# Kernel tuning notes

Hardware: AMD Instinct MI355X
Metric: run time of the kernel (lower is better)

## Reference

```python
import jax, jax.numpy as jnp
import numpy as np

B, S, SE = 4, 1024, 1024
E, H, M = 768, 12, 100
D = E // H
EPS = 1e-5
GELU_C = 0.7978845608028654  # sqrt(2/pi)


def _ln(x, g, b):
    mu = x.mean(-1, keepdims=True)
    v = ((x - mu) ** 2).mean(-1, keepdims=True)
    return g * (x - mu) / jnp.sqrt(v + EPS) + b


def _gelu(x):
    return 0.5 * x * (1.0 + jnp.tanh(GELU_C * (x + 0.044715 * x ** 3)))


def _split(x):  # [b,s,E] -> [b,H,s,D]
    b, s, _ = x.shape
    return x.reshape(b, s, H, D).transpose(0, 2, 1, 3)


def _merge(x):  # [b,H,s,D] -> [b,s,E]
    b, h, s, d = x.shape
    return x.transpose(0, 2, 1, 3).reshape(b, s, h * d)


def _forward(x, encoder_features, ln1_g, ln1_b, ln2_g, ln2_b,
             c_attn_w, c_attn_b, attn_proj_w, attn_proj_b,
             memory_features, mem_attn_w, mem_attn_b, mem_alpha_w, mem_alpha_b,
             fcq_w, fcq_b, fck_w, fck_b, fcv_w, fcv_b, enc_proj_w, enc_proj_b,
             fc_alpha1_w, fc_alpha1_b, fc_alpha2_w, fc_alpha2_b,
             mlp_fc_w, mlp_fc_b, mlp_proj_w, mlp_proj_b, mask_encoder):
    # ---- memory-augmented self-attention (note: original has NO 1/sqrt(d) scaling here) ----
    h = _ln(x, ln1_g, ln1_b)
    qkv = h @ c_attn_w + c_attn_b
    q, k, v = jnp.split(qkv, 3, axis=-1)
    q, k, v = _split(q), _split(k), _split(v)
    w = jax.nn.softmax(jnp.einsum('bhqd,bhkd->bhqk', q, k), axis=-1)
    a = _merge(jnp.einsum('bhqk,bhkd->bhqd', w, v))
    # memory slots are batch-independent -> compute once, broadcast over batch
    mem = memory_features[0] @ mem_attn_w + mem_attn_b  # [M, 2E]
    mk, mv = jnp.split(mem, 2, axis=-1)
    mk = mk.reshape(M, H, D).transpose(1, 2, 0)  # [H,D,M]
    mv = mv.reshape(M, H, D).transpose(1, 0, 2)  # [H,M,D]
    wm = jax.nn.softmax(jnp.einsum('bhqd,hdm->bhqm', q, mk), axis=-1)
    a1 = _merge(jnp.einsum('bhqm,hmd->bhqd', wm, mv))
    al = jax.nn.sigmoid(jnp.concatenate([a, a1], -1) @ mem_alpha_w + mem_alpha_b)
    a = al * a + (1.0 - al) * a1
    a = a @ attn_proj_w + attn_proj_b
    a = x + a  # residual (dropout = identity in eval)

    # ---- two cross-attentions sharing weights and ln_1 ----
    ha = _ln(a, ln1_g, ln1_b)

    def enc_dec(enc):
        qe = _split(ha @ fcq_w + fcq_b)
        ke = _split(enc @ fck_w + fck_b)
        ve = _split(enc @ fcv_w + fcv_b)
        we = jnp.einsum('bhqd,bhkd->bhqk', qe, ke) / np.float32(np.sqrt(D))
        we = jnp.where(mask_encoder, jnp.float32(-10000.0), we)
        we = jax.nn.softmax(we, axis=-1)
        o = _merge(jnp.einsum('bhqk,bhkd->bhqd', we, ve))
        return o @ enc_proj_w + enc_proj_b

    e1 = enc_dec(_ln(encoder_features[:, 0], ln1_g, ln1_b))
    e2 = enc_dec(_ln(encoder_features[:, 1], ln1_g, ln1_b))
    al1 = jax.nn.sigmoid(jnp.concatenate([a, e1], -1) @ fc_alpha1_w + fc_alpha1_b)
    al2 = jax.nn.sigmoid(jnp.concatenate([a, e2], -1) @ fc_alpha2_w + fc_alpha2_b)
    e1 = al1 * a + (1.0 - al1) * e1
    e2 = al2 * a + (1.0 - al2) * e2
    a = (e1 + e2) / np.float32(np.sqrt(2.0))

    # ---- MLP ----
    hm = _ln(a, ln2_g, ln2_b)
    m = _gelu(hm @ mlp_fc_w + mlp_fc_b) @ mlp_proj_w + mlp_proj_b
    return a + m


def setup_inputs() -> dict:
    key = jax.random.key(0)
    ks = iter(jax.random.split(key, 48))

    def rn(shape, s=0.02):
        return jax.random.normal(next(ks), shape, jnp.float32) * s

    return dict(
        x=jax.random.normal(next(ks), (B, S, E), jnp.float32),
        encoder_features=jax.random.normal(next(ks), (B, 2, SE, E), jnp.float32),
        mask_encoder=jax.random.bernoulli(next(ks), 0.1, (B, 1, 1, SE)),
        ln1_g=jnp.ones(E, jnp.float32), ln1_b=jnp.zeros(E, jnp.float32),
        ln2_g=jnp.ones(E, jnp.float32), ln2_b=jnp.zeros(E, jnp.float32),
        c_attn_w=rn((E, 3 * E)), c_attn_b=jnp.zeros(3 * E, jnp.float32),
        attn_proj_w=rn((E, E)), attn_proj_b=jnp.zeros(E, jnp.float32),
        memory_features=rn((1, M, E), 1.0),
        mem_attn_w=rn((E, 2 * E)), mem_attn_b=jnp.zeros(2 * E, jnp.float32),
        mem_alpha_w=rn((2 * E, E)), mem_alpha_b=jnp.zeros(E, jnp.float32),
        fcq_w=rn((E, E)), fcq_b=jnp.zeros(E, jnp.float32),
        fck_w=rn((E, E)), fck_b=jnp.zeros(E, jnp.float32),
        fcv_w=rn((E, E)), fcv_b=jnp.zeros(E, jnp.float32),
        enc_proj_w=rn((E, E)), enc_proj_b=jnp.zeros(E, jnp.float32),
        fc_alpha1_w=rn((2 * E, E)), fc_alpha1_b=jnp.zeros(E, jnp.float32),
        fc_alpha2_w=rn((2 * E, E)), fc_alpha2_b=jnp.zeros(E, jnp.float32),
        mlp_fc_w=rn((E, 4 * E)), mlp_fc_b=jnp.zeros(4 * E, jnp.float32),
        mlp_proj_w=rn((4 * E, E)), mlp_proj_b=jnp.zeros(E, jnp.float32),
    )


def reference(x, encoder_features, mask_encoder, ln1_g, ln1_b, ln2_g, ln2_b,
              c_attn_w, c_attn_b, attn_proj_w, attn_proj_b,
              memory_features, mem_attn_w, mem_attn_b, mem_alpha_w, mem_alpha_b,
              fcq_w, fcq_b, fck_w, fck_b, fcv_w, fcv_b, enc_proj_w, enc_proj_b,
              fc_alpha1_w, fc_alpha1_b, fc_alpha2_w, fc_alpha2_b,
              mlp_fc_w, mlp_fc_b, mlp_proj_w, mlp_proj_b):
    return _forward(x, encoder_features, ln1_g, ln1_b, ln2_g, ln2_b,
                    c_attn_w, c_attn_b, attn_proj_w, attn_proj_b,
                    memory_features, mem_attn_w, mem_attn_b, mem_alpha_w, mem_alpha_b,
                    fcq_w, fcq_b, fck_w, fck_b, fcv_w, fcv_b, enc_proj_w, enc_proj_b,
                    fc_alpha1_w, fc_alpha1_b, fc_alpha2_w, fc_alpha2_b,
                    mlp_fc_w, mlp_fc_b, mlp_proj_w, mlp_proj_b, mask_encoder)
```

## Files before the change

### kernel.cpp

```cpp
#include <hip/hip_runtime.h>

typedef __bf16 bf16_t;
typedef __bf16 bf16x8v __attribute__((ext_vector_type(8)));
typedef float f32x4 __attribute__((ext_vector_type(4)));

#define CB 4
#define CE 768
#define CH 12
#define CD 64

__device__ __forceinline__ float fexp2(float x) { return __builtin_amdgcn_exp2f(x); }

__device__ __forceinline__ void gload16(const void* g, void* l) {
    __builtin_amdgcn_global_load_lds((const __attribute__((address_space(1))) void*)g,
                                     (__attribute__((address_space(3))) void*)l, 16, 0, 0);
}

__device__ __forceinline__ void xcd_remap(int& bx, int& by, int gx, int gy) {
    int nwg = gx * gy;
    if ((nwg & 7) == 0) {
        int lin = by * gx + bx;
        int lin2 = (lin & 7) * (nwg >> 3) + (lin >> 3);
        bx = lin2 % gx;
        by = lin2 / gx;
    }
}

template<int BM, int BN, int CONCAT, int ACT, int RES, int OUT, int CMODE>
__global__ __launch_bounds__(256)
void gemm_n(const bf16_t* __restrict__ A0, const bf16_t* __restrict__ A1,
            const bf16_t* __restrict__ Bt, const float* __restrict__ bias,
            const float* __restrict__ bias2, const void* __restrict__ resid,
            void* __restrict__ C, void* __restrict__ C2, void* __restrict__ C3,
            int M, int N, int K, int lda, int ldc)
{
    constexpr int WM = BM / 2, WN = BN / 2, RM = WM / 16, RN = WN / 16;
    __shared__ __align__(16) bf16_t As0[BM * 64], As1[BM * 64];
    __shared__ __align__(16) bf16_t Bs0[BN * 64], Bs1[BN * 64];

    const int t = threadIdx.x;
    const int lane = t & 63, wave = t >> 6;
    int bx = blockIdx.x, by = blockIdx.y;
    xcd_remap(bx, by, gridDim.x, gridDim.y);
    const int m0 = by * BM, n0 = bx * BN;
    const int wm = (wave & 1) * WM, wn = (wave >> 1) * WN;
    const int fr = lane & 15, quad = lane >> 4;

    const int lr = lane >> 3;
    const int kof = ((lane & 7) ^ lr) * 8;

    const bf16_t* A1b = A1;
    if (CMODE == 6) A1b = A1 + (n0 >= 768 ? (long)4096 * 768 : 0);

    f32x4 acc[RM][RN];
#pragma unroll
    for (int i = 0; i < RM; i++)
#pragma unroll
        for (int j = 0; j < RN; j++)
#pragma unroll
            for (int p = 0; p < 4; p++) acc[i][j][p] = 0.f;

    auto stage = [&](bf16_t* As, bf16_t* Bs, int kt) {
        const bf16_t* Ab = A0;
        int kk = kt;
        if (CONCAT && kt >= 768) { Ab = A1b; kk = kt - 768; }
        const bf16_t* asrc = Ab + (long)(m0 + wave * 8 + lr) * lda + kk + kof;
#pragma unroll
        for (int c = 0; c < BM / 32; ++c)
            gload16(asrc + (long)c * 32 * lda, &As[(c * 32 + wave * 8) * 64]);
        const bf16_t* bsrc = Bt + (long)(n0 + wave * 8 + lr) * K + kt + kof;
#pragma unroll
        for (int c = 0; c < BN / 32; ++c)
            gload16(bsrc + (long)c * 32 * K, &Bs[(c * 32 + wave * 8) * 64]);
    };

    const int sw = fr & 7;
    auto compute = [&](const bf16_t* As, const bf16_t* Bs) {
        bf16x8v af[RM][2], bfr[RN][2];
        const int s0 = quad ^ sw;
#pragma unroll
        for (int i = 0; i < RM; ++i) {
            const char* rb = (const char*)As + (wm + i * 16 + fr) * 128;
            af[i][0] = *(const bf16x8v*)(rb + (s0 << 4));
            af[i][1] = *(const bf16x8v*)(rb + ((s0 ^ 4) << 4));
        }
#pragma unroll
        for (int j = 0; j < RN; ++j) {
            const char* rb = (const char*)Bs + (wn + j * 16 + fr) * 128;
            bfr[j][0] = *(const bf16x8v*)(rb + (s0 << 4));
            bfr[j][1] = *(const bf16x8v*)(rb + ((s0 ^ 4) << 4));
        }
#pragma unroll
        for (int ks = 0; ks < 2; ++ks)
#pragma unroll
            for (int i = 0; i < RM; ++i)
#pragma unroll
                for (int j = 0; j < RN; ++j)
                    acc[i][j] = __builtin_amdgcn_mfma_f32_16x16x32_bf16(af[i][ks], bfr[j][ks], acc[i][j], 0, 0, 0);
    };

    const int nk = K >> 6;
    stage(As0, Bs0, 0);
    __syncthreads();
    for (int kt = 0; kt + 2 <= nk; kt += 2) {
        stage(As1, Bs1, (kt + 1) << 6);
        compute(As0, Bs0);
        __syncthreads();
        if (kt + 2 < nk) stage(As0, Bs0, (kt + 2) << 6);
        compute(As1, Bs1);
        __syncthreads();
    }

    const int rq = quad * 4, cn = fr;
#pragma unroll
    for (int i = 0; i < RM; i++)
#pragma unroll
        for (int j = 0; j < RN; j++) {
            int col = n0 + wn + j * 16 + cn;
            int t3 = (CMODE == 4 || CMODE == 5) ? (col / 768) : 0;
            int cc = col - t3 * 768;
            float bv = 0.f;
            if (CMODE == 5)      bv = t3 ? bias2[cc] : bias[cc];
            else if (CMODE == 6) bv = (col < 768) ? bias[col] : bias2[col - 768];
            else if (bias)       bv = bias[col];
            const int row0 = m0 + wm + i * 16 + rq;
            float vv[4];
#pragma unroll
            for (int p = 0; p < 4; p++) {
                float v = acc[i][j][p] + bv;
                if (ACT == 1) v = 1.f / (1.f + __expf(-v));
                if (ACT == 2) {
                    float u2 = 1.5957691216057308f * (v + 0.044715f * v * v * v);
                    v = v / (1.f + __expf(-u2));
                }
                if (RES == 2) v += ((const float*)resid)[(long)(row0 + p) * ldc + col];
                vv[p] = v;
            }
            if (CMODE == 0) {
#pragma unroll
                for (int p = 0; p < 4; p++) {
                    long idx = (long)(row0 + p) * ldc + col;
                    if (OUT == 0)      ((bf16_t*)C)[idx] = (bf16_t)vv[p];
                    else if (OUT == 1) ((float*)C)[idx] = vv[p];
                    else { ((float*)C)[idx] = vv[p]; ((bf16_t*)C2)[idx] = (bf16_t)vv[p]; }
                }
            } else if (CMODE == 6) {
                long base = (col < 768) ? 0 : ((long)4096 * 768 - 768);
#pragma unroll
                for (int p = 0; p < 4; p++)
                    ((bf16_t*)C)[base + (long)(row0 + p) * 768 + col] = (bf16_t)vv[p];
            } else {
                int bb = row0 >> 10, ss0 = row0 & 1023;
                int hh = cc >> 6, dd = cc & 63;
                long srow = (long)(bb * CH + hh) * 1024 + ss0;
                long tbase = (((long)(bb * CH + hh) * 64) + dd) * 1024 + ss0;
                union { ushort4 u4; bf16_t b[4]; } pk;
#pragma unroll
                for (int p = 0; p < 4; p++) pk.b[p] = (bf16_t)vv[p];
                if (CMODE == 2) {
#pragma unroll
                    for (int p = 0; p < 4; p++)
                        ((bf16_t*)C)[(srow + p) * 64 + dd] = pk.b[p];
                } else if (CMODE == 5) {
                    if (t3 == 0) {
#pragma unroll
                        for (int p = 0; p < 4; p++)
                            ((bf16_t*)C)[(srow + p) * 64 + dd] = pk.b[p];
                    } else {
                        *(ushort4*)((bf16_t*)C2 + tbase) = pk.u4;
                    }
                } else {
                    if (t3 == 0) {
#pragma unroll
                        for (int p = 0; p < 4; p++)
                            ((bf16_t*)C)[(srow + p) * 64 + dd] = pk.b[p];
                    } else if (t3 == 1) {
#pragma unroll
                        for (int p = 0; p < 4; p++)
                            ((bf16_t*)C2)[(srow + p) * 64 + dd] = pk.b[p];
                    } else {
                        *(ushort4*)((bf16_t*)C3 + tbase) = pk.u4;
                    }
                }
            }
        }
}

template<int MODE>
__global__ __launch_bounds__(256)
void flash_attn(const bf16_t* __restrict__ Q, const bf16_t* __restrict__ K,
                const bf16_t* __restrict__ V, const int* __restrict__ mask,
                bf16_t* __restrict__ O)
{
    __shared__ __align__(16) bf16_t Qs[64 * 72];
    __shared__ __align__(16) bf16_t Ks0[64 * 64], Ks1[64 * 64];
    __shared__ __align__(16) bf16_t Vs[64 * 64];

    const int t = threadIdx.x;
    const int lane = t & 63, wave = t >> 6;
    int bx = blockIdx.x, bz = blockIdx.z;
    {
        int nwg = gridDim.x * gridDim.z;
        if ((nwg & 7) == 0) {
            int lin = bz * gridDim.x + bx;
            int lin2 = (lin & 7) * (nwg >> 3) + (lin >> 3);
            bx = lin2 % gridDim.x;
            bz = lin2 / gridDim.x;
        }
    }
    const int zq = (MODE == 1) ? (bz % 48) : bz;
    const int b = zq / CH, h = bz % CH;
    const long eoff = (MODE == 1) ? (long)(bz / 48) * ((long)4096 * 768) : 0;
    const int q0 = bx * 64;

    const bf16_t* Qb = Q + (long)zq * 65536 + (long)q0 * 64;
    const bf16_t* Kb = (MODE == 2) ? K + (long)h * (128 * 64) : K + (long)bz * 65536;
    const bf16_t* Vb = (MODE == 2) ? V + (long)h * (64 * 128) : V + (long)bz * 65536;
    const int ldv = (MODE == 2) ? 128 : 1024;
    const int NT = (MODE == 2) ? 2 : 16;
    constexpr float SCL = (MODE == 1) ? 0.18033688011112042f : 1.4426950408889634f;

    const int lr = lane >> 3, kof = ((lane & 7) ^ lr) * 8;

    auto stageK = [&](bf16_t* Ks, int kt) {
#pragma unroll
        for (int c = 0; c < 2; ++c) {
            int r = wave * 8 + c * 32;
            gload16(Kb + (long)(kt * 64 + r + lr) * 64 + kof, &Ks[r * 64]);
        }
    };
    auto stageV = [&](int kt) {
#pragma unroll
        for (int c = 0; c < 2; ++c) {
            int r = wave * 8 + c * 32;
            gload16(Vb + (long)(r + lr) * ldv + kt * 64 + kof, &Vs[r * 64]);
        }
    };

    stageK(Ks0, 0);
    const int r0 = t >> 3, c0 = (t & 7) * 8;
    for (int rr = r0; rr < 64; rr += 32)
        *(uint4*)&Qs[rr * 72 + c0] = *(const uint4*)&Qb[(long)rr * 64 + c0];
    __syncthreads();

    const int fr = lane & 15, quad = lane >> 4;
    const int sw = fr & 7;
    bf16x8v qf[2];
#pragma unroll
    for (int ks = 0; ks < 2; ks++) {
        bf16x8v raw = *(const bf16x8v*)&Qs[(wave * 16 + fr) * 72 + quad * 8 + ks * 32];
#pragma unroll
        for (int i = 0; i < 8; i++) qf[ks][i] = (bf16_t)((float)raw[i] * SCL);
    }

    bf16_t* Ps = &Qs[wave * 16 * 72];

    f32x4 o[4];
    float mrow = -1e30f, lrow = 0.f;
#pragma unroll
    for (int j = 0; j < 4; j++)
#pragma unroll
        for (int p = 0; p < 4; p++) o[j][p] = 0.f;

    auto qkt_sm = [&](const bf16_t* Ks, int kt) {
        f32x4 s[4];
#pragma unroll
        for (int j = 0; j < 4; j++)
#pragma unroll
            for (int p = 0; p < 4; p++) s[j][p] = 0.f;
        __builtin_amdgcn_s_setprio(1);
#pragma unroll
        for (int ks = 0; ks < 2; ks++) {
            bf16x8v bk[4];
#pragma unroll
            for (int j = 0; j < 4; j++) {
                const char* rb = (const char*)Ks + (j * 16 + fr) * 128;
                bk[j] = *(const bf16x8v*)(rb + (((quad ^ sw) ^ (ks << 2)) << 4));
            }
#pragma unroll
            for (int j = 0; j < 4; j++)
                s[j] = __builtin_amdgcn_mfma_f32_16x16x32_bf16(bk[j], qf[ks], s[j], 0, 0, 0);
        }
        __builtin_amdgcn_s_setprio(0);
        if (MODE == 1) {
#pragma unroll
            for (int j = 0; j < 4; j++) {
                int4 mv = *(const int4*)&mask[(long)b * 1024 + kt * 64 + j * 16 + quad * 4];
                s[j][0] = mv.x ? -14426.95f : s[j][0];
                s[j][1] = mv.y ? -14426.95f : s[j][1];
                s[j][2] = mv.z ? -14426.95f : s[j][2];
                s[j][3] = mv.w ? -14426.95f : s[j][3];
            }
        }
        if (MODE == 2) {
#pragma unroll
            for (int j = 0; j < 4; j++)
#pragma unroll
                for (int p = 0; p < 4; p++)
                    if (kt * 64 + j * 16 + quad * 4 + p >= 100) s[j][p] = -1e30f;
        }
        float tm = s[0][0];
#pragma unroll
        for (int j = 0; j < 4; j++)
#pragma unroll
            for (int p = 0; p < 4; p++) tm = fmaxf(tm, s[j][p]);
        tm = fmaxf(tm, __shfl_xor(tm, 16, 64));
        tm = fmaxf(tm, __shfl_xor(tm, 32, 64));
        bool need = tm > mrow + 8.f;
        if (__any(need ? 1 : 0)) {
            float mnew = fmaxf(mrow, tm);
            float alpha = fexp2(mrow - mnew);
            lrow *= alpha;
            mrow = mnew;
            float arow[4];
#pragma unroll
            for (int p = 0; p < 4; p++)
                arow[p] = __shfl(alpha, (lane & 48) | (quad * 4 + p), 64);
#pragma unroll
            for (int j = 0; j < 4; j++)
#pragma unroll
                for (int p = 0; p < 4; p++) o[j][p] *= arow[p];
        }
        float rs = 0.f;
#pragma unroll
        for (int j = 0; j < 4; j++)
#pragma unroll
            for (int p = 0; p < 4; p++) {
                float e = fexp2(s[j][p] - mrow);
                s[j][p] = e;
                rs += e;
            }
        rs += __shfl_xor(rs, 16, 64);
        rs += __shfl_xor(rs, 32, 64);
        lrow += rs;
#pragma unroll
        for (int j = 0; j < 4; j++) {
            union { uint2 u; bf16_t bb[4]; } pk;
#pragma unroll
            for (int p = 0; p < 4; p++) pk.bb[p] = (bf16_t)s[j][p];
            *(uint2*)&Ps[fr * 72 + j * 16 + quad * 4] = pk.u;
        }
    };

    auto pv = [&]() {
        __builtin_amdgcn_s_setprio(1);
#pragma unroll
        for (int ks = 0; ks < 2; ks++) {
            bf16x8v af = *(const bf16x8v*)&Ps[fr * 72 + quad * 8 + ks * 32];
            bf16x8v bv[4];
#pragma unroll
            for (int j = 0; j < 4; j++) {
                const char* rb = (const char*)Vs + (j * 16 + fr) * 128;
                bv[j] = *(const bf16x8v*)(rb + (((quad ^ sw) ^ (ks << 2)) << 4));
            }
#pragma unroll
            for (int j = 0; j < 4; j++)
                o[j] = __builtin_amdgcn_mfma_f32_16x16x32_bf16(af, bv[j], o[j], 0, 0, 0);
        }
        __builtin_amdgcn_s_setprio(0);
    };

    for (int kt = 0; kt < NT; kt += 2) {
        stageV(kt);
        if (kt + 1 < NT) stageK(Ks1, kt + 1);
        qkt_sm(Ks0, kt);
        __syncthreads();
        pv();
        __syncthreads();
        stageV(kt + 1);
        if (kt + 2 < NT) stageK(Ks0, kt + 2);
        qkt_sm(Ks1, kt + 1);
        __syncthreads();
        pv();
        __syncthreads();
    }
    float linv[4];
#pragma unroll
    for (int p = 0; p < 4; p++)
        linv[p] = 1.f / __shfl(lrow, (lane & 48) | (quad * 4 + p), 64);
#pragma unroll
    for (int p = 0; p < 4; p++) {
        int srow = q0 + wave * 16 + quad * 4 + p;
        long base = ((long)b * 1024 + srow) * 768 + h * 64 + eoff;
#pragma unroll
        for (int j = 0; j < 4; j++)
            O[base + j * 16 + fr] = (bf16_t)(o[j][p] * linv[p]);
    }
}

__device__ __forceinline__ void ln_body(const float* in, bf16_t* out,
                                        const float* g, const float* b,
                                        long base, long ob, int t)
{
    __shared__ float red[4];
    float v0 = in[base + t], v1 = in[base + t + 256], v2 = in[base + t + 512];
    float s = v0 + v1 + v2;
    for (int m = 32; m; m >>= 1) s += __shfl_xor(s, m, 64);
    if ((t & 63) == 0) red[t >> 6] = s;
    __syncthreads();
    s = red[0] + red[1] + red[2] + red[3];
    __syncthreads();
    const float mu = s * (1.f / 768.f);
    float d0 = v0 - mu, d1 = v1 - mu, d2 = v2 - mu;
    float q = d0 * d0 + d1 * d1 + d2 * d2;
    for (int m = 32; m; m >>= 1) q += __shfl_xor(q, m, 64);
    if ((t & 63) == 0) red[t >> 6] = q;
    __syncthreads();
    q = red[0] + red[1] + red[2] + red[3];
    const float rstd = rsqrtf(q * (1.f / 768.f) + 1e-5f);
    out[ob + t]       = (bf16_t)(g[t]       * d0 * rstd + b[t]);
    out[ob + t + 256] = (bf16_t)(g[t + 256] * d1 * rstd + b[t + 256]);
    out[ob + t + 512] = (bf16_t)(g[t + 512] * d2 * rstd + b[t + 512]);
}

__global__ __launch_bounds__(256)
void ln_kernel(const float* __restrict__ in, bf16_t* __restrict__ out,
               const float* __restrict__ g, const float* __restrict__ b)
{
    const int r = blockIdx.x;
    ln_body(in, out, g, b, (long)r * CE, (long)r * CE, threadIdx.x);
}

__global__ __launch_bounds__(256)
void ln_enc(const float* __restrict__ encf, bf16_t* __restrict__ out,
            const float* __restrict__ g, const float* __restrict__ b)
{
    const int r = blockIdx.x;
    const int e = r >> 12, rr = r & 4095, bb = rr >> 10, s = rr & 1023;
    ln_body(encf, out, g, b, ((long)(bb * 2 + e) * 1024 + s) * CE, (long)r * CE, threadIdx.x);
}

__global__ void blend_kernel(const bf16_t* __restrict__ al, bf16_t* __restrict__ a,
                             const bf16_t* __restrict__ a1)
{
    int idx = blockIdx.x * 256 + threadIdx.x;
    float g = (float)al[idx];
    a[idx] = (bf16_t)(g * (float)a[idx] + (1.f - g) * (float)a1[idx]);
}

__global__ void fuse_gates2(const bf16_t* __restrict__ gal, const bf16_t* __restrict__ eo,
                            float* __restrict__ rf)
{
    const long SZel = (long)4096 * 768;
    long idx = (long)blockIdx.x * 256 + threadIdx.x;
    float g1 = (float)gal[idx], g2 = (float)gal[idx + SZel];
    float e1 = (float)eo[idx],  e2 = (float)eo[idx + SZel];
    float r = rf[idx];
    float v = g1 * r + (1.f - g1) * e1 + g2 * r + (1.f - g2) * e2;
    rf[idx] = v * 0.7071067811865476f;
}

__global__ void zero_out(float* __restrict__ out)
{
    out[blockIdx.x * 256 + threadIdx.x] = 0.f;
}

__global__ void transpose_cast(const float* __restrict__ in, bf16_t* __restrict__ out,
                               int K, int N)
{
    __shared__ bf16_t tile[32][33];
    int n0 = blockIdx.x * 32, k0 = blockIdx.y * 32;
    int tx = threadIdx.x, ty = threadIdx.y;
    for (int i = ty; i < 32; i += 8)
        tile[i][tx] = (bf16_t)in[(long)(k0 + i) * N + n0 + tx];
    __syncthreads();
    for (int i = ty; i < 32; i += 8)
        out[(long)(n0 + i) * K + k0 + tx] = tile[tx][i];
}

__global__ void cast_pad_mem(const float* __restrict__ memf, bf16_t* __restrict__ out)
{
    int idx = blockIdx.x * 256 + threadIdx.x;
    int row = idx / 768;
    out[idx] = (row < 100) ? (bf16_t)memf[idx] : (bf16_t)0.f;
}

__global__ void repack_mem(const bf16_t* __restrict__ mem, bf16_t* __restrict__ mkt,
                           bf16_t* __restrict__ mvt)
{
    int idx = blockIdx.x * 256 + threadIdx.x;
    int d = idx & 63;
    int slot = (idx >> 6) & 127;
    int h = idx >> 13;
    bf16_t kv = (slot < 100) ? mem[slot * 1536 + h * CD + d] : (bf16_t)0.f;
    bf16_t vv = (slot < 100) ? mem[slot * 1536 + CE + h * CD + d] : (bf16_t)0.f;
    mkt[idx] = kv;
    mvt[((long)h * 64 + d) * 128 + slot] = vv;
}

extern "C" void kernel_launch(void* const* d_in, const int* in_sizes, int n_in,
                              void* d_out, int out_size, void* d_ws, size_t ws_size,
                              hipStream_t stream)
{
    (void)in_sizes; (void)n_in; (void)out_size;
    const float* x        = (const float*)d_in[0];
    const float* encf     = (const float*)d_in[1];
    const int*   maskenc  = (const int*)d_in[2];
    const float* ln1_g    = (const float*)d_in[3];
    const float* ln1_b    = (const float*)d_in[4];
    const float* ln2_g    = (const float*)d_in[5];
    const float* ln2_b    = (const float*)d_in[6];
    const float* c_attn_w = (const float*)d_in[7];
    const float* c_attn_b = (const float*)d_in[8];
    const float* aproj_w  = (const float*)d_in[9];
    const float* aproj_b  = (const float*)d_in[10];
    const float* memf     = (const float*)d_in[11];
    const float* mattn_w  = (const float*)d_in[12];
    const float* mattn_b  = (const float*)d_in[13];
    const float* malpha_w = (const float*)d_in[14];
    const float* malpha_b = (const float*)d_in[15];
    const float* fcq_w    = (const float*)d_in[16];
    const float* fcq_b    = (const float*)d_in[17];
    const float* fck_w    = (const float*)d_in[18];
    const float* fck_b    = (const float*)d_in[19];
    const float* fcv_w    = (const float*)d_in[20];
    const float* fcv_b    = (const float*)d_in[21];
    const float* eproj_w  = (const float*)d_in[22];
    const float* eproj_b  = (const float*)d_in[23];
    const float* fa1_w    = (const float*)d_in[24];
    const float* fa1_b    = (const float*)d_in[25];
    const float* fa2_w    = (const float*)d_in[26];
    const float* fa2_b    = (const float*)d_in[27];
    const float* mfc_w    = (const float*)d_in[28];
    const float* mfc_b    = (const float*)d_in[29];
    const float* mproj_w  = (const float*)d_in[30];
    const float* mproj_b  = (const float*)d_in[31];
    float* dout = (float*)d_out;

    size_t off = 0;
    auto alloc = [&](size_t bytes) -> void* {
        void* p = (char*)d_ws + off;
        off = (off + bytes + 255) & ~(size_t)255;
        return p;
    };
    const size_t SZ = (size_t)4096 * 768 * 2;
    const long SZel = (long)4096 * 768;
    bf16_t* wt_cattn  = (bf16_t*)alloc((size_t)2304 * 768 * 2);
    bf16_t* wt_aproj  = (bf16_t*)alloc((size_t)768 * 768 * 2);
    bf16_t* wt_malpha = (bf16_t*)alloc((size_t)768 * 1536 * 2);
    bf16_t* wt_fcq    = (bf16_t*)alloc((size_t)768 * 768 * 2);
    bf16_t* wt_fck    = (bf16_t*)alloc((size_t)768 * 768 * 2);
    bf16_t* wt_fcv    = (bf16_t*)alloc((size_t)768 * 768 * 2);
    bf16_t* wt_eproj  = (bf16_t*)alloc((size_t)768 * 768 * 2);
    bf16_t* wt_fa1    = (bf16_t*)alloc((size_t)768 * 1536 * 2);
    bf16_t* wt_fa2    = (bf16_t*)alloc((size_t)768 * 1536 * 2);
    bf16_t* wt_mfc    = (bf16_t*)alloc((size_t)3072 * 768 * 2);
    bf16_t* wt_mproj  = (bf16_t*)alloc((size_t)768 * 3072 * 2);
    bf16_t* wt_mattn  = (bf16_t*)alloc((size_t)1536 * 768 * 2);
    bf16_t* memb   = (bf16_t*)alloc((size_t)128 * 768 * 2);
    bf16_t* membuf = (bf16_t*)alloc((size_t)128 * 1536 * 2);
    bf16_t* mkt    = (bf16_t*)alloc((size_t)CH * 128 * 64 * 2);
    bf16_t* mvt    = (bf16_t*)alloc((size_t)CH * 64 * 128 * 2);
    bf16_t* bufA   = (bf16_t*)alloc(SZ);
    bf16_t* qbuf   = (bf16_t*)alloc(SZ);
    bf16_t* kbuf   = (bf16_t*)alloc(2 * SZ);
    bf16_t* vtbuf  = (bf16_t*)alloc(2 * SZ);
    bf16_t* asbuf  = (bf16_t*)alloc(2 * SZ);
    bf16_t* bufB   = (bf16_t*)alloc(2 * SZ);
    float*  residf = (float*)alloc((size_t)4096 * 768 * 4);
    bf16_t* residb = (bf16_t*)alloc(SZ);

    if (off > ws_size) {
        zero_out<<<12288, 256, 0, stream>>>(dout);
        return;
    }
    bf16_t* mid = kbuf;
    bf16_t* galbuf = kbuf;
    bf16_t* eobuf = bufB;

    const dim3 blk(256);

    auto T = [&](const float* w, bf16_t* wt, int Kd, int Nd) {
        transpose_cast<<<dim3(Nd / 32, Kd / 32), dim3(32, 8), 0, stream>>>(w, wt, Kd, Nd);
    };
    T(c_attn_w, wt_cattn, 768, 2304);
    T(aproj_w, wt_aproj, 768, 768);
    T(malpha_w, wt_malpha, 1536, 768);
    T(fcq_w, wt_fcq, 768, 768);
    T(fck_w, wt_fck, 768, 768);
    T(fcv_w, wt_fcv, 768, 768);
    T(eproj_w, wt_eproj, 768, 768);
    T(fa1_w, wt_fa1, 1536, 768);
    T(fa2_w, wt_fa2, 1536, 768);
    T(mfc_w, wt_mfc, 768, 3072);
    T(mproj_w, wt_mproj, 3072, 768);
    T(mattn_w, wt_mattn, 768, 1536);

    cast_pad_mem<<<384, blk, 0, stream>>>(memf, memb);
    gemm_n<64,64,0,0,0,0,0><<<dim3(24, 2), blk, 0, stream>>>(
        memb, nullptr, wt_mattn, mattn_b, nullptr, nullptr, membuf, nullptr, nullptr,
        128, 1536, 768, 768, 1536);
    repack_mem<<<384, blk, 0, stream>>>(membuf, mkt, mvt);

    ln_kernel<<<4096, blk, 0, stream>>>(x, bufA, ln1_g, ln1_b);
    gemm_n<128,128,0,0,0,0,4><<<dim3(18, 32), blk, 0, stream>>>(
        bufA, nullptr, wt_cattn, c_attn_b, nullptr, nullptr, qbuf, kbuf, vtbuf,
        4096, 2304, 768, 768, 0);

    flash_attn<0><<<dim3(16, 1, 48), blk, 0, stream>>>(qbuf, kbuf, vtbuf, nullptr, asbuf);
    flash_attn<2><<<dim3(16, 1, 48), blk, 0, stream>>>(qbuf, mkt, mvt, nullptr, asbuf + SZel);

    gemm_n<128,64,1,1,0,0,0><<<dim3(12, 32), blk, 0, stream>>>(
        asbuf, asbuf + SZel, wt_malpha, malpha_b, nullptr, nullptr, bufA, nullptr, nullptr,
        4096, 768, 1536, 768, 768);
    blend_kernel<<<12288, blk, 0, stream>>>(bufA, asbuf, asbuf + SZel);
    gemm_n<128,64,0,0,2,2,0><<<dim3(12, 32), blk, 0, stream>>>(
        asbuf, nullptr, wt_aproj, aproj_b, nullptr, x, residf, residb, nullptr,
        4096, 768, 768, 768, 768);

    ln_kernel<<<4096, blk, 0, stream>>>(residf, bufA, ln1_g, ln1_b);
    gemm_n<128,64,0,0,0,0,2><<<dim3(12, 32), blk, 0, stream>>>(
        bufA, nullptr, wt_fcq, fcq_b, nullptr, nullptr, qbuf, nullptr, nullptr,
        4096, 768, 768, 768, 0);

    ln_enc<<<8192, blk, 0, stream>>>(encf, bufB, ln1_g, ln1_b);
    gemm_n<128,128,0,0,0,0,5><<<dim3(12, 64), blk, 0, stream>>>(
        bufB, nullptr, wt_fck, fck_b, fcv_b, nullptr, kbuf, vtbuf, nullptr,
        8192, 1536, 768, 768, 0);
    flash_attn<1><<<dim3(16, 1, 96), blk, 0, stream>>>(
        qbuf, kbuf, vtbuf, maskenc, asbuf);
    gemm_n<128,128,0,0,0,0,0><<<dim3(6, 64), blk, 0, stream>>>(
        asbuf, nullptr, wt_eproj, eproj_b, nullptr, nullptr, eobuf, nullptr, nullptr,
        8192, 768, 768, 768, 768);
    gemm_n<128,64,1,1,0,0,6><<<dim3(24, 32), blk, 0, stream>>>(
        residb, eobuf, wt_fa1, fa1_b, fa2_b, nullptr, galbuf, nullptr, nullptr,
        4096, 1536, 1536, 768, 768);
    fuse_gates2<<<12288, blk, 0, stream>>>(galbuf, eobuf, residf);

    ln_kernel<<<4096, blk, 0, stream>>>(residf, bufA, ln2_g, ln2_b);
    gemm_n<128,128,0,2,0,0,0><<<dim3(24, 32), blk, 0, stream>>>(
        bufA, nullptr, wt_mfc, mfc_b, nullptr, nullptr, mid, nullptr, nullptr,
        4096, 3072, 768, 768, 3072);
    gemm_n<128,64,0,0,2,1,0><<<dim3(12, 32), blk, 0, stream>>>(
        mid, nullptr, wt_mproj, mproj_b, nullptr, residf, dout, nullptr, nullptr,
        4096, 768, 3072, 3072, 768);
}
```

Before: 600.5 us.

## Fuse gate blend into alpha GEMM epilogue and widen cross-attention query tiles

Adds a GEMM epilogue mode that applies the sigmoid-gated blend of the two attention outputs directly, which removes the separate blend kernel and one full round trip of the activations. Flash attention is templated on query rows per block, so each wave can process two 16-row query groups against each staged K/V tile. Cross-attention now uses 128 query rows per block, halving the K/V loads per query. Q is also loaded into a swizzled LDS layout via async global-to-LDS copies. The cost is more registers per thread and half as many blocks for the cross-attention launch, which may reduce occupancy.

```diff
diff --git a/kernel.cpp b/kernel.cpp
--- a/kernel.cpp
+++ b/kernel.cpp
@@ -149,6 +149,14 @@
 #pragma unroll
                 for (int p = 0; p < 4; p++)
                     ((bf16_t*)C)[base + (long)(row0 + p) * 768 + col] = (bf16_t)vv[p];
+            } else if (CMODE == 7) {
+#pragma unroll
+                for (int p = 0; p < 4; p++) {
+                    long idx = (long)(row0 + p) * ldc + col;
+                    float a  = (float)((const bf16_t*)C2)[idx];
+                    float a1 = (float)((const bf16_t*)C3)[idx];
+                    ((bf16_t*)C)[idx] = (bf16_t)(vv[p] * a + (1.f - vv[p]) * a1);
+                }
             } else {
                 int bb = row0 >> 10, ss0 = row0 & 1023;
                 int hh = cc >> 6, dd = cc & 63;
@@ -186,13 +194,14 @@
         }
 }
 
-template<int MODE>
+template<int MODE, int QR>
 __global__ __launch_bounds__(256)
 void flash_attn(const bf16_t* __restrict__ Q, const bf16_t* __restrict__ K,
                 const bf16_t* __restrict__ V, const int* __restrict__ mask,
                 bf16_t* __restrict__ O)
 {
-    __shared__ __align__(16) bf16_t Qs[64 * 72];
+    constexpr int QG = QR / 64;
+    __shared__ __align__(16) bf16_t Qs[QR * 64];
     __shared__ __align__(16) bf16_t Ks0[64 * 64], Ks1[64 * 64];
     __shared__ __align__(16) bf16_t Vs[64 * 64];
 
@@ -211,7 +220,7 @@
     const int zq = (MODE == 1) ? (bz % 48) : bz;
     const int b = zq / CH, h = bz % CH;
     const long eoff = (MODE == 1) ? (long)(bz / 48) * ((long)4096 * 768) : 0;
-    const int q0 = bx * 64;
+    const int q0 = bx * QR;
 
     const bf16_t* Qb = Q + (long)zq * 65536 + (long)q0 * 64;
     const bf16_t* Kb = (MODE == 2) ? K + (long)h * (128 * 64) : K + (long)bz * 65536;
@@ -238,36 +247,47 @@
     };
 
     stageK(Ks0, 0);
-    const int r0 = t >> 3, c0 = (t & 7) * 8;
-    for (int rr = r0; rr < 64; rr += 32)
-        *(uint4*)&Qs[rr * 72 + c0] = *(const uint4*)&Qb[(long)rr * 64 + c0];
+#pragma unroll
+    for (int c = 0; c < QR / 32; ++c) {
+        int r = wave * 8 + c * 32;
+        gload16(Qb + (long)(r + lr) * 64 + kof, &Qs[r * 64]);
+    }
     __syncthreads();
 
     const int fr = lane & 15, quad = lane >> 4;
     const int sw = fr & 7;
-    bf16x8v qf[2];
-#pragma unroll
-    for (int ks = 0; ks < 2; ks++) {
-        bf16x8v raw = *(const bf16x8v*)&Qs[(wave * 16 + fr) * 72 + quad * 8 + ks * 32];
-#pragma unroll
-        for (int i = 0; i < 8; i++) qf[ks][i] = (bf16_t)((float)raw[i] * SCL);
-    }
-
-    bf16_t* Ps = &Qs[wave * 16 * 72];
-
-    f32x4 o[4];
-    float mrow = -1e30f, lrow = 0.f;
+    bf16x8v qf[QG][2];
+#pragma unroll
+    for (int g = 0; g < QG; g++)
+#pragma unroll
+        for (int ks = 0; ks < 2; ks++) {
+            const char* rb = (const char*)Qs + (wave * (16 * QG) + g * 16 + fr) * 128;
+            bf16x8v raw = *(const bf16x8v*)(rb + (((quad ^ sw) ^ (ks << 2)) << 4));
+#pragma unroll
+            for (int i = 0; i < 8; i++) qf[g][ks][i] = (bf16_t)((float)raw[i] * SCL);
+        }
+
+    bf16_t* Ps = &Qs[wave * (16 * QG) * 64];
+
+    f32x4 o[4][QG];
+    float mrow[QG], lrow[QG];
+#pragma unroll
+    for (int g = 0; g < QG; g++) { mrow[g] = -1e30f; lrow[g] = 0.f; }
 #pragma unroll
     for (int j = 0; j < 4; j++)
 #pragma unroll
-        for (int p = 0; p < 4; p++) o[j][p] = 0.f;
+        for (int g = 0; g < QG; g++)
+#pragma unroll
+            for (int p = 0; p < 4; p++) o[j][g][p] = 0.f;
 
     auto qkt_sm = [&](const bf16_t* Ks, int kt) {
-        f32x4 s[4];
+        f32x4 s[4][QG];
 #pragma unroll
         for (int j = 0; j < 4; j++)
 #pragma unroll
-            for (int p = 0; p < 4; p++) s[j][p] = 0.f;
+            for (int g = 0; g < QG; g++)
+#pragma unroll
+                for (int p = 0; p < 4; p++) s[j][g][p] = 0.f;
         __builtin_amdgcn_s_setprio(1);
 #pragma unroll
         for (int ks = 0; ks < 2; ks++) {
@@ -279,17 +299,22 @@
             }
 #pragma unroll
             for (int j = 0; j < 4; j++)
-                s[j] = __builtin_amdgcn_mfma_f32_16x16x32_bf16(bk[j], qf[ks], s[j], 0, 0, 0);
+#pragma unroll
+                for (int g = 0; g < QG; g++)
+                    s[j][g] = __builtin_amdgcn_mfma_f32_16x16x32_bf16(bk[j], qf[g][ks], s[j][g], 0, 0, 0);
         }
         __builtin_amdgcn_s_setprio(0);
         if (MODE == 1) {
 #pragma unroll
             for (int j = 0; j < 4; j++) {
                 int4 mv = *(const int4*)&mask[(long)b * 1024 + kt * 64 + j * 16 + quad * 4];
-                s[j][0] = mv.x ? -14426.95f : s[j][0];
-                s[j][1] = mv.y ? -14426.95f : s[j][1];
-                s[j][2] = mv.z ? -14426.95f : s[j][2];
-                s[j][3] = mv.w ? -14426.95f : s[j][3];
+#pragma unroll
+                for (int g = 0; g < QG; g++) {
+                    s[j][g][0] = mv.x ? -14426.95f : s[j][g][0];
+                    s[j][g][1] = mv.y ? -14426.95f : s[j][g][1];
+                    s[j][g][2] = mv.z ? -14426.95f : s[j][g][2];
+                    s[j][g][3] = mv.w ? -14426.95f : s[j][g][3];
+                }
             }
         }
         if (MODE == 2) {
@@ -297,57 +322,79 @@
             for (int j = 0; j < 4; j++)
 #pragma unroll
                 for (int p = 0; p < 4; p++)
-                    if (kt * 64 + j * 16 + quad * 4 + p >= 100) s[j][p] = -1e30f;
-        }
-        float tm = s[0][0];
+                    if (kt * 64 + j * 16 + quad * 4 + p >= 100)
+#pragma unroll
+                        for (int g = 0; g < QG; g++) s[j][g][p] = -1e30f;
+        }
+        float tmax[QG];
+        bool need = false;
+#pragma unroll
+        for (int g = 0; g < QG; g++) {
+            float tm = s[0][g][0];
+#pragma unroll
+            for (int j = 0; j < 4; j++)
+#pragma unroll
+                for (int p = 0; p < 4; p++) tm = fmaxf(tm, s[j][g][p]);
+            tm = fmaxf(tm, __shfl_xor(tm, 16, 64));
+            tm = fmaxf(tm, __shfl_xor(tm, 32, 64));
+            tmax[g] = tm;
+            need = need || (tm > mrow[g] + 8.f);
+        }
+        if (__any(need ? 1 : 0)) {
+#pragma unroll
+            for (int g = 0; g < QG; g++) {
+                float mnew = fmaxf(mrow[g], tmax[g]);
+                float alpha = fexp2(mrow[g] - mnew);
+                lrow[g] *= alpha;
+                mrow[g] = mnew;
+                float arow[4];
+#pragma unroll
+                for (int p = 0; p < 4; p++)
+                    arow[p] = __shfl(alpha, (lane & 48) | (quad * 4 + p), 64);
+#pragma unroll
+                for (int j = 0; j < 4; j++)
+#pragma unroll
+                    for (int p = 0; p < 4; p++) o[j][g][p] *= arow[p];
+            }
+        }
+#pragma unroll
+        for (int g = 0; g < QG; g++) {
+            float rs = 0.f;
+#pragma unroll
+            for (int j = 0; j < 4; j++)
+#pragma unroll
+                for (int p = 0; p < 4; p++) {
+                    float e = fexp2(s[j][g][p] - mrow[g]);
+                    s[j][g][p] = e;
+                    rs += e;
+                }
+            rs += __shfl_xor(rs, 16, 64);
+            rs += __shfl_xor(rs, 32, 64);
+            lrow[g] += rs;
+        }
 #pragma unroll
         for (int j = 0; j < 4; j++)
 #pragma unroll
-            for (int p = 0; p < 4; p++) tm = fmaxf(tm, s[j][p]);
-        tm = fmaxf(tm, __shfl_xor(tm, 16, 64));
-        tm = fmaxf(tm, __shfl_xor(tm, 32, 64));
-        bool need = tm > mrow + 8.f;
-        if (__any(need ? 1 : 0)) {
-            float mnew = fmaxf(mrow, tm);
-            float alpha = fexp2(mrow - mnew);
-            lrow *= alpha;
-            mrow = mnew;
-            float arow[4];
-#pragma unroll
-            for (int p = 0; p < 4; p++)
-                arow[p] = __shfl(alpha, (lane & 48) | (quad * 4 + p), 64);
-#pragma unroll
-            for (int j = 0; j < 4; j++)
-#pragma unroll
-                for (int p = 0; p < 4; p++) o[j][p] *= arow[p];
-        }
-        float rs = 0.f;
-#pragma unroll
-        for (int j = 0; j < 4; j++)
-#pragma unroll
-            for (int p = 0; p < 4; p++) {
-                float e = fexp2(s[j][p] - mrow);
-                s[j][p] = e;
-                rs += e;
-            }
-        rs += __shfl_xor(rs, 16, 64);
-        rs += __shfl_xor(rs, 32, 64);
-        lrow += rs;
-#pragma unroll
-        for (int j = 0; j < 4; j++) {
-            union { uint2 u; bf16_t bb[4]; } pk;
-#pragma unroll
-            for (int p = 0; p < 4; p++) pk.bb[p] = (bf16_t)s[j][p];
-            *(uint2*)&Ps[fr * 72 + j * 16 + quad * 4] = pk.u;
-        }
+            for (int g = 0; g < QG; g++) {
+                union { uint2 u; bf16_t bb[4]; } pk;
+#pragma unroll
+                for (int p = 0; p < 4; p++) pk.bb[p] = (bf16_t)s[j][g][p];
+                int row = g * 16 + fr;
+                *(uint2*)((char*)Ps + row * 128 +
+                          (((j * 2 + (quad >> 1)) ^ sw) << 4) + ((quad & 1) << 3)) = pk.u;
+            }
     };
 
     auto pv = [&]() {
         __builtin_amdgcn_s_setprio(1);
 #pragma unroll
         for (int ks = 0; ks < 2; ks++) {
-            bf16x8v af = *(const bf16x8v*)&Ps[fr * 72 + quad * 8 + ks * 32];
-            bf16x8v bv[4];
+            bf16x8v af[QG], bv[4];
+#pragma unroll
+            for (int g = 0; g < QG; g++) {
+                const char* rb = (const char*)Ps + (g * 16 + fr) * 128;
+                af[g] = *(const bf16x8v*)(rb + (((quad ^ sw) ^ (ks << 2)) << 4));
+            }
 #pragma unroll
             for (int j = 0; j < 4; j++) {
                 const char* rb = (const char*)Vs + (j * 16 + fr) * 128;
@@ -355,7 +402,9 @@
             }
 #pragma unroll
             for (int j = 0; j < 4; j++)
-                o[j] = __builtin_amdgcn_mfma_f32_16x16x32_bf16(af, bv[j], o[j], 0, 0, 0);
+#pragma unroll
+                for (int g = 0; g < QG; g++)
+                    o[j][g] = __builtin_amdgcn_mfma_f32_16x16x32_bf16(af[g], bv[j], o[j][g], 0, 0, 0);
         }
         __builtin_amdgcn_s_setprio(0);
     };
@@ -374,17 +423,20 @@
         pv();
         __syncthreads();
     }
-    float linv[4];
-#pragma unroll
-    for (int p = 0; p < 4; p++)
-        linv[p] = 1.f / __shfl(lrow, (lane & 48) | (quad * 4 + p), 64);
-#pragma unroll
-    for (int p = 0; p < 4; p++) {
-        int srow = q0 + wave * 16 + quad * 4 + p;
-        long base = ((long)b * 1024 + srow) * 768 + h * 64 + eoff;
-#pragma unroll
-        for (int j = 0; j < 4; j++)
-            O[base + j * 16 + fr] = (bf16_t)(o[j][p] * linv[p]);
+#pragma unroll
+    for (int g = 0; g < QG; g++) {
+        float linv[4];
+#pragma unroll
+        for (int p = 0; p < 4; p++)
+            linv[p] = 1.f / __shfl(lrow[g], (lane & 48) | (quad * 4 + p), 64);
+#pragma unroll
+        for (int p = 0; p < 4; p++) {
+            int srow = q0 + wave * (16 * QG) + g * 16 + quad * 4 + p;
+            long base = ((long)b * 1024 + srow) * 768 + h * 64 + eoff;
+#pragma unroll
+            for (int j = 0; j < 4; j++)
+                O[base + j * 16 + fr] = (bf16_t)(o[j][g][p] * linv[p]);
+        }
     }
 }
 
@@ -428,14 +480,6 @@
     const int r = blockIdx.x;
     const int e = r >> 12, rr = r & 4095, bb = rr >> 10, s = rr & 1023;
     ln_body(encf, out, g, b, ((long)(bb * 2 + e) * 1024 + s) * CE, (long)r * CE, threadIdx.x);
-}
-
-__global__ void blend_kernel(const bf16_t* __restrict__ al, bf16_t* __restrict__ a,
-                             const bf16_t* __restrict__ a1)
-{
-    int idx = blockIdx.x * 256 + threadIdx.x;
-    float g = (float)al[idx];
-    a[idx] = (bf16_t)(g * (float)a[idx] + (1.f - g) * (float)a1[idx]);
 }
 
 __global__ void fuse_gates2(const bf16_t* __restrict__ gal, const bf16_t* __restrict__ eo,
@@ -597,15 +641,14 @@
         bufA, nullptr, wt_cattn, c_attn_b, nullptr, nullptr, qbuf, kbuf, vtbuf,
         4096, 2304, 768, 768, 0);
 
-    flash_attn<0><<<dim3(16, 1, 48), blk, 0, stream>>>(qbuf, kbuf, vtbuf, nullptr, asbuf);
-    flash_attn<2><<<dim3(16, 1, 48), blk, 0, stream>>>(qbuf, mkt, mvt, nullptr, asbuf + SZel);
-
-    gemm_n<128,64,1,1,0,0,0><<<dim3(12, 32), blk, 0, stream>>>(
-        asbuf, asbuf + SZel, wt_malpha, malpha_b, nullptr, nullptr, bufA, nullptr, nullptr,
+    flash_attn<0,64><<<dim3(16, 1, 48), blk, 0, stream>>>(qbuf, kbuf, vtbuf, nullptr, asbuf);
+    flash_attn<2,64><<<dim3(16, 1, 48), blk, 0, stream>>>(qbuf, mkt, mvt, nullptr, asbuf + SZel);
+
+    gemm_n<128,64,1,1,0,0,7><<<dim3(12, 32), blk, 0, stream>>>(
+        asbuf, asbuf + SZel, wt_malpha, malpha_b, nullptr, nullptr, bufA, asbuf, asbuf + SZel,
         4096, 768, 1536, 768, 768);
-    blend_kernel<<<12288, blk, 0, stream>>>(bufA, asbuf, asbuf + SZel);
     gemm_n<128,64,0,0,2,2,0><<<dim3(12, 32), blk, 0, stream>>>(
-        asbuf, nullptr, wt_aproj, aproj_b, nullptr, x, residf, residb, nullptr,
+        bufA, nullptr, wt_aproj, aproj_b, nullptr, x, residf, residb, nullptr,
         4096, 768, 768, 768, 768);
 
     ln_kernel<<<4096, blk, 0, stream>>>(residf, bufA, ln1_g, ln1_b);
@@ -617,7 +660,7 @@
     gemm_n<128,128,0,0,0,0,5><<<dim3(12, 64), blk, 0, stream>>>(
         bufB, nullptr, wt_fck, fck_b, fcv_b, nullptr, kbuf, vtbuf, nullptr,
         8192, 1536, 768, 768, 0);
-    flash_attn<1><<<dim3(16, 1, 96), blk, 0, stream>>>(
+    flash_attn<1,128><<<dim3(8, 1, 96), blk, 0, stream>>>(
         qbuf, kbuf, vtbuf, maskenc, asbuf);
     gemm_n<128,128,0,0,0,0,0><<<dim3(6, 64), blk, 0, stream>>>(
         asbuf, nullptr, wt_eproj, eproj_b, nullptr, nullptr, eobuf, nullptr, nullptr,
```

After: 593.4 us. Within noise of the previous version (-1.2%).
